# Performance work log

Hardware: AMD Instinct MI355X
Metric: run time of the kernel (lower is better)

Reference implementation:

```python
import jax, jax.numpy as jnp
import numpy as np

N, E, G = 100000, 1600000, 64
IN_DIM, EMB, HID, HEADS, OUT = 128, 128, 32, 4, 64
CAT = HID * HEADS  # 128
EPS = 1e-5
SLOPE = 0.2


def gat_conv(x, src, dst, W, a_src, a_dst, bias):
    # x: [N, F_in]; W: [HEADS*HID, F_in]; a_*: [1, HEADS, HID]; bias: [HEADS*HID]
    h = (x @ W.T).reshape(N, HEADS, HID)
    s_src = (h * a_src).sum(-1)  # [N, HEADS]
    s_dst = (h * a_dst).sum(-1)
    e = jax.nn.leaky_relu(s_src[src] + s_dst[dst], SLOPE)  # [Etot, HEADS]
    m = jax.ops.segment_max(e, dst, num_segments=N)
    p = jnp.exp(e - m[dst])
    denom = jax.ops.segment_sum(p, dst, num_segments=N)
    alpha = p / denom[dst]  # softmax over incoming edges per dst node
    out = jax.ops.segment_sum(h[src] * alpha[:, :, None], dst, num_segments=N)
    return out.reshape(N, CAT) + bias


def graph_norm(x, batch, w, b, mean_scale):
    cnt = jax.ops.segment_sum(jnp.ones((N,), x.dtype), batch, num_segments=G)[:, None]
    mean = jax.ops.segment_sum(x, batch, num_segments=G) / cnt  # [G, C]
    sub = x - mean_scale * mean[batch]
    var = jax.ops.segment_sum(sub * sub, batch, num_segments=G) / cnt
    inv = 1.0 / jnp.sqrt(var + EPS)
    return w * sub * inv[batch] + b


def setup_inputs() -> dict:
    key = jax.random.key(0)
    ks = jax.random.split(key, 20)
    g = lambda k, shape, s: jax.random.normal(k, shape, dtype=jnp.float32) * s
    inp = {
        'x': g(ks[0], (N, IN_DIM), 1.0),
        'edge_index': jax.random.randint(ks[1], (2, E), 0, N, dtype=jnp.int64 if jax.config.read('jax_enable_x64') else jnp.int32),
        'batch': jnp.sort(jax.random.randint(ks[2], (N,), 0, G)),
        'enc_w': g(ks[3], (EMB, IN_DIM), 0.08),
        'enc_b': jnp.zeros((EMB,), jnp.float32),
        'w1': g(ks[4], (HEADS * HID, EMB), 0.08),
        'att_src1': g(ks[5], (1, HEADS, HID), 0.15),
        'att_dst1': g(ks[6], (1, HEADS, HID), 0.15),
        'b1': jnp.zeros((CAT,), jnp.float32),
        'n1_w': jnp.ones((CAT,), jnp.float32),
        'n1_b': jnp.zeros((CAT,), jnp.float32),
        'n1_ms': jnp.ones((CAT,), jnp.float32),
        'w2': g(ks[7], (HEADS * HID, CAT), 0.08),
        'att_src2': g(ks[8], (1, HEADS, HID), 0.15),
        'att_dst2': g(ks[9], (1, HEADS, HID), 0.15),
        'b2': jnp.zeros((CAT,), jnp.float32),
        'n2_w': jnp.ones((CAT,), jnp.float32),
        'n2_b': jnp.zeros((CAT,), jnp.float32),
        'n2_ms': jnp.ones((CAT,), jnp.float32),
        'fc_w': g(ks[10], (OUT, CAT), 0.08),
        'fc_b': jnp.zeros((OUT,), jnp.float32),
    }
    return inp


def reference(x, edge_index, batch, enc_w, enc_b, w1, att_src1, att_dst1, b1,
              n1_w, n1_b, n1_ms, w2, att_src2, att_dst2, b2, n2_w, n2_b, n2_ms,
              fc_w, fc_b):
    # PyG GATConv adds self-loops by default
    loops = jnp.arange(N, dtype=edge_index.dtype)
    src = jnp.concatenate([edge_index[0], loops])
    dst = jnp.concatenate([edge_index[1], loops])

    h = x @ enc_w.T + enc_b
    h = jax.nn.elu(gat_conv(h, src, dst, w1, att_src1, att_dst1, b1))
    h = graph_norm(h, batch, n1_w, n1_b, n1_ms)  # dropout = identity (eval)
    h = jax.nn.elu(gat_conv(h, src, dst, w2, att_src2, att_dst2, b2))
    h = graph_norm(h, batch, n2_w, n2_b, n2_ms)
    pooled = jax.ops.segment_max(h, batch, num_segments=G)  # global_max_pool
    return pooled @ fc_w.T + fc_b  # out_dim != 1 -> no sigmoid
```

## Files before the change

### kernel.cpp

```cpp
#include <hip/hip_runtime.h>
#include <hip/hip_bf16.h>

#define SLOPE 0.2f
#define EPS_GN 1e-5f
#define APITCH 136
#define NBUCK 391

typedef __attribute__((ext_vector_type(8))) short bfrag;
typedef __attribute__((ext_vector_type(4))) float ffrag;

__device__ __forceinline__ float lrelu(float v) { return v > 0.f ? v : SLOPE * v; }
__device__ __forceinline__ short f2bs(float v) {
    __hip_bfloat16 h = __float2bfloat16(v);
    return *reinterpret_cast<short*>(&h);
}
__device__ __forceinline__ float blo(unsigned int u) { return __uint_as_float(u << 16); }
__device__ __forceinline__ float bhi(unsigned int u) { return __uint_as_float(u & 0xffff0000u); }


__global__ void __launch_bounds__(256) bucket_hist(
    const int* __restrict__ ei, int* __restrict__ bhist,
    const float* __restrict__ enc_w, const float* __restrict__ enc_b,
    const float* __restrict__ w1, const float* __restrict__ w2,
    unsigned short* __restrict__ WT1b, unsigned short* __restrict__ WT2b,
    float* __restrict__ bc1, float* __restrict__ bc2, int E, int N) {
    __shared__ int h[NBUCK];
    __shared__ float w1row[128];
    int t = threadIdx.x, bid = blockIdx.x;
    for (int i = t; i < NBUCK; i += 256) h[i] = 0;
    bool prep = (bid < 128) && (t < 128);
    if (prep) w1row[t] = w1[bid * 128 + t];
    __syncthreads();
    int base = bid * 4096;
#pragma unroll
    for (int s = 0; s < 16; ++s) {
        int e = base + s * 256 + t;
        if (e < E + N) {
            int dst = (e < E) ? ei[E + e] : (e - E);
            atomicAdd(&h[dst >> 8], 1);
        }
    }
    if (prep) {
        float acc = 0.f;
        for (int j = 0; j < 128; ++j)
            acc = fmaf(w1row[j], enc_w[j * 128 + t], acc);
        WT1b[bid * 128 + t] = (unsigned short)f2bs(acc);
        WT2b[bid * 128 + t] = (unsigned short)f2bs(w2[bid * 128 + t]);
        if (t == 0) {
            float b = 0.f;
            for (int j = 0; j < 128; ++j) b += w1row[j] * enc_b[j];
            bc1[bid] = b;
            bc2[bid] = 0.f;
        }
    }
    __syncthreads();
    for (int i = t; i < NBUCK; i += 256)
        if (h[i]) atomicAdd(&bhist[i], h[i]);
}

__global__ void bucket_scan(const int* __restrict__ bhist,
                            int* __restrict__ bbase, int* __restrict__ bcur) {
    __shared__ int sh[512];
    int t = threadIdx.x;
    int v = (t < NBUCK) ? bhist[t] : 0;
    sh[t] = v;
    __syncthreads();
    for (int off = 1; off < 512; off <<= 1) {
        int add = (t >= off) ? sh[t - off] : 0;
        __syncthreads();
        sh[t] += add;
        __syncthreads();
    }
    if (t < NBUCK) {
        bbase[t] = sh[t] - v;
        bcur[t] = sh[t] - v;
    }
}

__global__ void __launch_bounds__(256) bucket_scatter(const int* __restrict__ ei,
                                                      int* __restrict__ bcur,
                                                      unsigned int* __restrict__ staging,
                                                      int E, int N) {
    __shared__ int h[NBUCK];
    __shared__ int lb[NBUCK];
    for (int i = threadIdx.x; i < NBUCK; i += 256) h[i] = 0;
    __syncthreads();
    int base = blockIdx.x * 4096;
    int srcv[16], dstv[16];
#pragma unroll
    for (int s = 0; s < 16; ++s) {
        int e = base + s * 256 + threadIdx.x;
        srcv[s] = -1;
        if (e < E + N) {
            srcv[s] = (e < E) ? ei[e] : (e - E);
            dstv[s] = (e < E) ? ei[E + e] : (e - E);
            atomicAdd(&h[dstv[s] >> 8], 1);
        }
    }
    __syncthreads();
    for (int i = threadIdx.x; i < NBUCK; i += 256) {
        int c = h[i];
        lb[i] = c ? atomicAdd(&bcur[i], c) : 0;
        h[i] = 0;
    }
    __syncthreads();
#pragma unroll
    for (int s = 0; s < 16; ++s) {
        if (srcv[s] >= 0) {
            int b = dstv[s] >> 8;
            int slot = atomicAdd(&h[b], 1);
            staging[lb[b] + slot] = ((unsigned int)srcv[s] << 8) | (unsigned int)(dstv[s] & 255);
        }
    }
}

__global__ void __launch_bounds__(256) bucket_finalize(
    const unsigned int* __restrict__ staging,
    const int* __restrict__ bbase, const int* __restrict__ bcur,
    int* __restrict__ rowp, int* __restrict__ esrc, int N, int Etot) {
    int b = blockIdx.x, t = threadIdx.x;
    __shared__ int h[256], sc[256];
    h[t] = 0;
    __syncthreads();
    int s0 = bbase[b], s1 = bcur[b];
    for (int j = s0 + t; j < s1; j += 256)
        atomicAdd(&h[staging[j] & 255], 1);
    __syncthreads();
    int d = h[t];
    sc[t] = d;
    __syncthreads();
    for (int off = 1; off < 256; off <<= 1) {
        int add = (t >= off) ? sc[t - off] : 0;
        __syncthreads();
        sc[t] += add;
        __syncthreads();
    }
    int excl = s0 + sc[t] - d;
    int node = b * 256 + t;
    if (node < N) rowp[node] = excl;
    if (b == 0 && t == 0) rowp[N] = Etot;
    __syncthreads();
    h[t] = excl;
    __syncthreads();
    for (int j = s0 + t; j < s1; j += 256) {
        unsigned int p = staging[j];
        int pos = atomicAdd(&h[p & 255], 1);
        esrc[pos] = (int)(p >> 8);
    }
}

__global__ void __launch_bounds__(256) gemm_mfma(
    const void* __restrict__ Ain, const unsigned short* __restrict__ WTb,
    const float* __restrict__ bias, const float* __restrict__ att_src,
    const float* __restrict__ att_dst, const int* __restrict__ batch,
    const float* __restrict__ Ac, const float* __restrict__ Bc,
    unsigned int* __restrict__ H, float* __restrict__ ssrc, float* __restrict__ sdst, int N) {
    __shared__ __align__(16) short Bsh[128 * APITCH];
    __shared__ __align__(16) short Ash[64 * APITCH];
    int tid = threadIdx.x;
    int base = blockIdx.x * 64;

    int lane = tid & 63, col = lane & 15, quad = lane >> 4;
    int w = tid >> 6;
    int rowBase = w * 16;

    float2 av = *(const float2*)&att_src[lane * 2];
    float2 dv = *(const float2*)&att_dst[lane * 2];
    float bvr[8];
#pragma unroll
    for (int t = 0; t < 8; ++t) bvr[t] = bias[t * 16 + col];

    for (int idx = tid; idx < 2048; idx += 256) {
        int c = idx >> 4, k8 = (idx & 15) * 8;
        uint4 wv = ((const uint4*)WTb)[idx];
        *(uint4*)&Bsh[c * APITCH + k8] = wv;
    }
    if (Ac == nullptr) {
        const float* A = (const float*)Ain;
        for (int idx = tid; idx < 2048; idx += 256) {
            int nl = idx >> 5, k4 = (idx & 31) * 4;
            int node = base + nl;
            float4 v = make_float4(0.f, 0.f, 0.f, 0.f);
            if (node < N) v = ((const float4*)A)[node * 32 + (idx & 31)];
            *(short4*)&Ash[nl * APITCH + k4] =
                make_short4(f2bs(v.x), f2bs(v.y), f2bs(v.z), f2bs(v.w));
        }
    } else {
        const uint4* A4 = (const uint4*)Ain;
        for (int idx = tid; idx < 1024; idx += 256) {
            int nl = idx >> 4, u4 = idx & 15, k8 = u4 * 8;
            int node = base + nl;
            short o[8] = {0, 0, 0, 0, 0, 0, 0, 0};
            if (node < N) {
                uint4 hb = A4[node * 16 + u4];
                int g = batch[node];
                float4 a0 = *(const float4*)&Ac[g * 128 + k8];
                float4 a1 = *(const float4*)&Ac[g * 128 + k8 + 4];
                float4 b0 = *(const float4*)&Bc[g * 128 + k8];
                float4 b1 = *(const float4*)&Bc[g * 128 + k8 + 4];
                o[0] = f2bs(fmaf(blo(hb.x), a0.x, b0.x));
                o[1] = f2bs(fmaf(bhi(hb.x), a0.y, b0.y));
                o[2] = f2bs(fmaf(blo(hb.y), a0.z, b0.z));
                o[3] = f2bs(fmaf(bhi(hb.y), a0.w, b0.w));
                o[4] = f2bs(fmaf(blo(hb.z), a1.x, b1.x));
                o[5] = f2bs(fmaf(bhi(hb.z), a1.y, b1.y));
                o[6] = f2bs(fmaf(blo(hb.w), a1.z, b1.z));
                o[7] = f2bs(fmaf(bhi(hb.w), a1.w, b1.w));
            }
            *(bfrag*)&Ash[nl * APITCH + k8] = *(bfrag*)o;
        }
    }
    __syncthreads();

    bfrag afr[4];
#pragma unroll
    for (int s = 0; s < 4; ++s)
        afr[s] = *(const bfrag*)&Ash[(rowBase + col) * APITCH + s * 32 + quad * 8];

    ffrag acc[8];
#pragma unroll
    for (int t = 0; t < 8; ++t) acc[t] = (ffrag){0.f, 0.f, 0.f, 0.f};

#pragma unroll
    for (int t = 0; t < 8; ++t) {
#pragma unroll
        for (int s = 0; s < 4; ++s) {
            bfrag bfr = *(const bfrag*)&Bsh[(t * 16 + col) * APITCH + s * 32 + quad * 8];
            acc[t] = __builtin_amdgcn_mfma_f32_16x16x32_bf16(afr[s], bfr, acc[t], 0, 0, 0);
        }
    }

#pragma unroll
    for (int t = 0; t < 8; ++t) {
        int ch = t * 16 + col;
        float bv = bvr[t];
#pragma unroll
        for (int r = 0; r < 4; ++r)
            Ash[(rowBase + quad * 4 + r) * APITCH + ch] = f2bs(acc[t][r] + bv);
    }
    __syncthreads();

    for (int r = 0; r < 16; ++r) {
        int node = base + rowBase + r;
        unsigned int hb = *(const unsigned int*)&Ash[(rowBase + r) * APITCH + lane * 2];
        float hx = blo(hb);
        float hy = bhi(hb);
        float vs = hx * av.x + hy * av.y;
        float vd = hx * dv.x + hy * dv.y;
#pragma unroll
        for (int off = 8; off; off >>= 1) {
            vs += __shfl_xor(vs, off, 16);
            vd += __shfl_xor(vd, off, 16);
        }
        if (node < N) {
            H[node * 64 + lane] = hb;
            if ((lane & 15) == 0) {
                int h = lane >> 4;
                ssrc[node * 4 + h] = vs;
                sdst[node * 4 + h] = vd;
            }
        }
    }
}

__global__ void __launch_bounds__(256) agg_kernel(
    const int* __restrict__ row, const int* __restrict__ esrc,
    const float* __restrict__ ssrc, const float* __restrict__ sdst,
    const uint4* __restrict__ H4, const float* __restrict__ bias,
    uint4* __restrict__ out, int N) {
    int n = (blockIdx.x * 256 + threadIdx.x) >> 6;
    int lane = threadIdx.x & 63;
    if (n >= N) return;
    int slot = lane >> 4, li = lane & 15, head = li >> 2;
    int beg = row[n], end = row[n + 1];
    int last = end - 1;
    float sdh = sdst[n * 4 + head];

    float num[8] = {0.f, 0.f, 0.f, 0.f, 0.f, 0.f, 0.f, 0.f};
    float den = 0.f;
    for (int ebase = beg; ebase < end; ebase += 20) {
        int sv[5];
        float av[5];
        uint4 hv[5];
        bool ok[5];
#pragma unroll
        for (int j = 0; j < 5; ++j) {
            int e = ebase + slot + 4 * j;
            ok[j] = (e < end);
            sv[j] = esrc[min(e, last)];
        }
#pragma unroll
        for (int j = 0; j < 5; ++j) {
            av[j] = ssrc[sv[j] * 4 + head];
            hv[j] = H4[sv[j] * 16 + li];
        }
        __builtin_amdgcn_sched_barrier(0);
#pragma unroll
        for (int j = 0; j < 5; ++j) {
            float al = ok[j] ? __expf(lrelu(av[j] + sdh)) : 0.f;
            den += al;
            num[0] = fmaf(al, blo(hv[j].x), num[0]);
            num[1] = fmaf(al, bhi(hv[j].x), num[1]);
            num[2] = fmaf(al, blo(hv[j].y), num[2]);
            num[3] = fmaf(al, bhi(hv[j].y), num[3]);
            num[4] = fmaf(al, blo(hv[j].z), num[4]);
            num[5] = fmaf(al, bhi(hv[j].z), num[5]);
            num[6] = fmaf(al, blo(hv[j].w), num[6]);
            num[7] = fmaf(al, bhi(hv[j].w), num[7]);
        }
    }
    den += __shfl_xor(den, 16);
    den += __shfl_xor(den, 32);
#pragma unroll
    for (int j = 0; j < 8; ++j) {
        num[j] += __shfl_xor(num[j], 16);
        num[j] += __shfl_xor(num[j], 32);
    }
    if (slot == 0) {
        float rh = 1.f / den;
        int c0 = li * 8;
        unsigned int o[4];
#pragma unroll
        for (int p = 0; p < 4; ++p) {
            float v0 = fmaf(num[2 * p], rh, bias[c0 + 2 * p]);
            float v1 = fmaf(num[2 * p + 1], rh, bias[c0 + 2 * p + 1]);
            v0 = v0 > 0.f ? v0 : __expf(v0) - 1.f;
            v1 = v1 > 0.f ? v1 : __expf(v1) - 1.f;
            o[p] = ((unsigned int)(unsigned short)f2bs(v0)) |
                   (((unsigned int)(unsigned short)f2bs(v1)) << 16);
        }
        out[n * 16 + li] = make_uint4(o[0], o[1], o[2], o[3]);
    }
}

template <int POOL>
__global__ void __launch_bounds__(256) stats_kernel(
    const uint4* __restrict__ X4, const int* __restrict__ batch,
    float* __restrict__ part, int N) {
    __shared__ float red[16][16][9];
    int t = threadIdx.x, u4 = t & 15, rg = t >> 4;
    int base = blockIdx.x * 64;
    int g0 = batch[base];

    float s[2][8] = {}, q[2][8] = {};
    float mx[2][8], mn[2][8];
#pragma unroll
    for (int st = 0; st < 2; ++st)
#pragma unroll
        for (int p = 0; p < 8; ++p) { mx[st][p] = -3e38f; mn[st][p] = 3e38f; }

#pragma unroll
    for (int rr = 0; rr < 4; ++rr) {
        int node = base + rg + rr * 16;
        if (node < N) {
            uint4 hb = X4[node * 16 + u4];
            int st = (batch[node] != g0) ? 1 : 0;
            float vv[8] = {blo(hb.x), bhi(hb.x), blo(hb.y), bhi(hb.y),
                           blo(hb.z), bhi(hb.z), blo(hb.w), bhi(hb.w)};
#pragma unroll
            for (int p = 0; p < 8; ++p) {
                s[st][p] += vv[p];
                q[st][p] += vv[p] * vv[p];
                if (POOL) {
                    mx[st][p] = fmaxf(mx[st][p], vv[p]);
                    mn[st][p] = fminf(mn[st][p], vv[p]);
                }
            }
        }
    }

    int uu = t >> 3, ch = t & 7;
    float rs[2] = {0.f, 0.f}, rq[2] = {0.f, 0.f};
    float rmx[2] = {-3e38f, -3e38f}, rmn[2] = {3e38f, 3e38f};
    for (int st = 0; st < 2; ++st) {
#pragma unroll
        for (int p = 0; p < 8; ++p) red[rg][u4][p] = s[st][p];
        __syncthreads();
        if (t < 128) { float a = 0.f; for (int r2 = 0; r2 < 16; ++r2) a += red[r2][uu][ch]; rs[st] = a; }
        __syncthreads();
#pragma unroll
        for (int p = 0; p < 8; ++p) red[rg][u4][p] = q[st][p];
        __syncthreads();
        if (t < 128) { float a = 0.f; for (int r2 = 0; r2 < 16; ++r2) a += red[r2][uu][ch]; rq[st] = a; }
        __syncthreads();
        if (POOL) {
#pragma unroll
            for (int p = 0; p < 8; ++p) red[rg][u4][p] = mx[st][p];
            __syncthreads();
            if (t < 128) { float a = -3e38f; for (int r2 = 0; r2 < 16; ++r2) a = fmaxf(a, red[r2][uu][ch]); rmx[st] = a; }
            __syncthreads();
#pragma unroll
            for (int p = 0; p < 8; ++p) red[rg][u4][p] = mn[st][p];
            __syncthreads();
            if (t < 128) { float a = 3e38f; for (int r2 = 0; r2 < 16; ++r2) a = fminf(a, red[r2][uu][ch]); rmn[st] = a; }
            __syncthreads();
        }
    }
    if (t < 128) {
        float* pb = part + (size_t)blockIdx.x * 8 * 128;
        pb[0 * 128 + t] = rs[0];
        pb[1 * 128 + t] = rq[0];
        pb[2 * 128 + t] = rs[1];
        pb[3 * 128 + t] = rq[1];
        if (POOL) {
            pb[4 * 128 + t] = rmx[0];
            pb[5 * 128 + t] = rmn[0];
            pb[6 * 128 + t] = rmx[1];
            pb[7 * 128 + t] = rmn[1];
        }
    }
}

__global__ void reduce_coef0(const float* __restrict__ part,
                             const int* __restrict__ batch, int N,
                             const float* __restrict__ w, const float* __restrict__ b,
                             const float* __restrict__ ms,
                             float* __restrict__ Ac, float* __restrict__ Bc) {
    __shared__ int sh2[2];
    int g = blockIdx.x, c = threadIdx.x;
    if (c < 2) {
        int key = g + c;
        int lo = 0, hi = N;
        while (lo < hi) { int m = (lo + hi) >> 1; if (batch[m] < key) lo = m + 1; else hi = m; }
        sh2[c] = lo;
    }
    __syncthreads();
    int sidx = sh2[0], eidx = sh2[1];
    float cnt = (float)(eidx - sidx);
    if (cnt < 0.5f) {
        Ac[g * 128 + c] = 0.f;
        Bc[g * 128 + c] = 0.f;
        return;
    }
    int b0 = sidx >> 6, b1 = (eidx - 1) >> 6;
    float s = 0.f, q = 0.f;
    for (int bb = b0; bb <= b1; ++bb) {
        int g0b = batch[bb << 6];
        int qoff;
        bool take;
        if (g0b == g) { qoff = 0; take = true; }
        else {
            int g1b = batch[min((bb << 6) + 63, N - 1)];
            take = (g1b == g);
            qoff = 2;
        }
        if (take) {
            const float* pb = part + (size_t)bb * 8 * 128;
            s += pb[qoff * 128 + c];
            q += pb[(qoff + 1) * 128 + c];
        }
    }
    float mean = s / cnt;
    float msv = ms[c];
    float var = q / cnt - msv * (2.f - msv) * mean * mean;
    var = fmaxf(var, 0.f);
    float inv = rsqrtf(var + EPS_GN);
    float a = w[c] * inv;
    float bb2 = b[c] - msv * mean * a;
    Ac[g * 128 + c] = a;
    Bc[g * 128 + c] = bb2;
}

__global__ void rc_fc(const float* __restrict__ part,
                      const int* __restrict__ batch, int N,
                      const float* __restrict__ w, const float* __restrict__ b,
                      const float* __restrict__ ms,
                      const float* __restrict__ fcw,
                      const float* __restrict__ fcb,
                      float* __restrict__ out) {
    __shared__ int sh2[2];
    __shared__ float prow[128];
    int g = blockIdx.x, c = threadIdx.x;
    if (c < 2) {
        int key = g + c;
        int lo = 0, hi = N;
        while (lo < hi) { int m = (lo + hi) >> 1; if (batch[m] < key) lo = m + 1; else hi = m; }
        sh2[c] = lo;
    }
    __syncthreads();
    int sidx = sh2[0], eidx = sh2[1];
    float cnt = (float)(eidx - sidx);
    float pooledv = 0.f;
    if (cnt >= 0.5f) {
        int b0 = sidx >> 6, b1 = (eidx - 1) >> 6;
        float s = 0.f, q = 0.f, M = -3e38f, m = 3e38f;
        for (int bb = b0; bb <= b1; ++bb) {
            int g0b = batch[bb << 6];
            int qoff;
            bool take;
            if (g0b == g) { qoff = 0; take = true; }
            else {
                int g1b = batch[min((bb << 6) + 63, N - 1)];
                take = (g1b == g);
                qoff = 2;
            }
            if (take) {
                const float* pb = part + (size_t)bb * 8 * 128;
                s += pb[qoff * 128 + c];
                q += pb[(qoff + 1) * 128 + c];
                M = fmaxf(M, pb[(4 + qoff) * 128 + c]);
                m = fminf(m, pb[(5 + qoff) * 128 + c]);
            }
        }
        float mean = s / cnt;
        float msv = ms[c];
        float var = q / cnt - msv * (2.f - msv) * mean * mean;
        var = fmaxf(var, 0.f);
        float inv = rsqrtf(var + EPS_GN);
        float a = w[c] * inv;
        float bb2 = b[c] - msv * mean * a;
        pooledv = (a >= 0.f) ? fmaf(a, M, bb2) : fmaf(a, m, bb2);
    }
    prow[c] = pooledv;
    __syncthreads();
    if (c < 64) {
        float acc = fcb[c];
        for (int k = 0; k < 128; ++k)
            acc = fmaf(prow[k], fcw[c * 128 + k], acc);
        out[g * 64 + c] = acc;
    }
}

extern "C" void kernel_launch(void* const* d_in, const int* in_sizes, int n_in,
                              void* d_out, int out_size, void* d_ws, size_t ws_size,
                              hipStream_t stream) {
    const float* x     = (const float*)d_in[0];
    const int* ei      = (const int*)d_in[1];
    const int* batch   = (const int*)d_in[2];
    const float* enc_w = (const float*)d_in[3];
    const float* enc_b = (const float*)d_in[4];
    const float* w1    = (const float*)d_in[5];
    const float* as1   = (const float*)d_in[6];
    const float* ad1   = (const float*)d_in[7];
    const float* b1    = (const float*)d_in[8];
    const float* n1w   = (const float*)d_in[9];
    const float* n1b   = (const float*)d_in[10];
    const float* n1ms  = (const float*)d_in[11];
    const float* w2    = (const float*)d_in[12];
    const float* as2   = (const float*)d_in[13];
    const float* ad2   = (const float*)d_in[14];
    const float* b2    = (const float*)d_in[15];
    const float* n2w   = (const float*)d_in[16];
    const float* n2b   = (const float*)d_in[17];
    const float* n2ms  = (const float*)d_in[18];
    const float* fcw   = (const float*)d_in[19];
    const float* fcb   = (const float*)d_in[20];
    float* out = (float*)d_out;

    int N = in_sizes[2];
    int E = in_sizes[1] / 2;
    int Etot = E + N;
    int SB = (N + 63) / 64;

    char* ws = (char*)d_ws;
    size_t off = 0;
    auto take = [&](size_t bytes) {
        char* p = ws + off;
        off = (off + bytes + 255) & ~(size_t)255;
        return p;
    };
    unsigned short* WT1b = (unsigned short*)take(128 * 128 * 2);
    unsigned short* WT2b = (unsigned short*)take(128 * 128 * 2);
    float* bc1 = (float*)take(512);
    float* bc2 = (float*)take(512);
    float* ssrc = (float*)take((size_t)N * 16);
    float* sdst = (float*)take((size_t)N * 16);
    int* rowp   = (int*)take((size_t)(N + 1) * 4);
    int* esrc   = (int*)take((size_t)Etot * 4);
    unsigned int* staging = (unsigned int*)take((size_t)Etot * 4);
    int* bbase  = (int*)take(512 * 4);
    int* bcur   = (int*)take(512 * 4);
    int* bhist  = (int*)take(512 * 4);
    unsigned int* H = (unsigned int*)take((size_t)N * 256);
    unsigned int* AG = (unsigned int*)take((size_t)N * 256);
    float* Ac   = (float*)take(64 * 128 * 4);
    float* Bc   = (float*)take(64 * 128 * 4);
    float* part = (float*)take((size_t)SB * 8 * 128 * 4);
    if (off > ws_size) return;

    int EB = (Etot + 4095) / 4096;

    hipMemsetAsync(bhist, 0, 512 * 4, stream);

    bucket_hist<<<EB, 256, 0, stream>>>(ei, bhist, enc_w, enc_b, w1, w2,
                                        WT1b, WT2b, bc1, bc2, E, N);
    bucket_scan<<<1, 512, 0, stream>>>(bhist, bbase, bcur);
    bucket_scatter<<<EB, 256, 0, stream>>>(ei, bcur, staging, E, N);
    bucket_finalize<<<NBUCK, 256, 0, stream>>>(staging, bbase, bcur, rowp, esrc, N, Etot);

    gemm_mfma<<<(N + 63) / 64, 256, 0, stream>>>(x, WT1b, bc1, as1, ad1, batch,
                                                 nullptr, nullptr, H, ssrc, sdst, N);
    agg_kernel<<<(N + 3) / 4, 256, 0, stream>>>(rowp, esrc, ssrc, sdst,
                                                (const uint4*)H, b1, (uint4*)AG, N);
    stats_kernel<0><<<SB, 256, 0, stream>>>((const uint4*)AG, batch, part, N);
    reduce_coef0<<<64, 128, 0, stream>>>(part, batch, N, n1w, n1b, n1ms, Ac, Bc);

    gemm_mfma<<<(N + 63) / 64, 256, 0, stream>>>(AG, WT2b, bc2, as2, ad2, batch,
                                                 Ac, Bc, H, ssrc, sdst, N);
    agg_kernel<<<(N + 3) / 4, 256, 0, stream>>>(rowp, esrc, ssrc, sdst,
                                                (const uint4*)H, b2, (uint4*)AG, N);
    stats_kernel<1><<<SB, 256, 0, stream>>>((const uint4*)AG, batch, part, N);
    rc_fc<<<64, 128, 0, stream>>>(part, batch, N, n2w, n2b, n2ms, fcw, fcb, out);
}
```

Before: 441.8 us.

## Fuse GAT aggregation with graph-norm statistics and skip final feature write

Merges the per-node attention aggregation kernel with the per-block graph-norm statistics kernel. Each block now handles 64 nodes, keeps the bf16 outputs in shared memory and reduces sum, sum-of-squares and max/min from there, so the aggregated features are not re-read from global memory. The second layer no longer writes its aggregated features at all, since only the statistics and pooled values are needed. The trade-off is fewer, larger blocks, with each wave processing 16 nodes in sequence, which can reduce the parallelism available to hide gather latency.

```diff
diff --git a/kernel.cpp b/kernel.cpp
--- a/kernel.cpp
+++ b/kernel.cpp
@@ -263,150 +263,121 @@
     }
 }
 
-__global__ void __launch_bounds__(256) agg_kernel(
+template <int POOL, int WROUT>
+__global__ void __launch_bounds__(256) agg_stats(
     const int* __restrict__ row, const int* __restrict__ esrc,
     const float* __restrict__ ssrc, const float* __restrict__ sdst,
     const uint4* __restrict__ H4, const float* __restrict__ bias,
-    uint4* __restrict__ out, int N) {
-    int n = (blockIdx.x * 256 + threadIdx.x) >> 6;
-    int lane = threadIdx.x & 63;
-    if (n >= N) return;
+    uint4* __restrict__ out, const int* __restrict__ batch,
+    float* __restrict__ part, int N) {
+    __shared__ unsigned int rows[64][64];
+    __shared__ int bsh[64];
+    int tid = threadIdx.x;
+    int lane = tid & 63, w = tid >> 6;
     int slot = lane >> 4, li = lane & 15, head = li >> 2;
-    int beg = row[n], end = row[n + 1];
-    int last = end - 1;
-    float sdh = sdst[n * 4 + head];
-
-    float num[8] = {0.f, 0.f, 0.f, 0.f, 0.f, 0.f, 0.f, 0.f};
-    float den = 0.f;
-    for (int ebase = beg; ebase < end; ebase += 20) {
-        int sv[5];
-        float av[5];
-        uint4 hv[5];
-        bool ok[5];
-#pragma unroll
-        for (int j = 0; j < 5; ++j) {
-            int e = ebase + slot + 4 * j;
-            ok[j] = (e < end);
-            sv[j] = esrc[min(e, last)];
-        }
-#pragma unroll
-        for (int j = 0; j < 5; ++j) {
-            av[j] = ssrc[sv[j] * 4 + head];
-            hv[j] = H4[sv[j] * 16 + li];
-        }
-        __builtin_amdgcn_sched_barrier(0);
-#pragma unroll
-        for (int j = 0; j < 5; ++j) {
-            float al = ok[j] ? __expf(lrelu(av[j] + sdh)) : 0.f;
-            den += al;
-            num[0] = fmaf(al, blo(hv[j].x), num[0]);
-            num[1] = fmaf(al, bhi(hv[j].x), num[1]);
-            num[2] = fmaf(al, blo(hv[j].y), num[2]);
-            num[3] = fmaf(al, bhi(hv[j].y), num[3]);
-            num[4] = fmaf(al, blo(hv[j].z), num[4]);
-            num[5] = fmaf(al, bhi(hv[j].z), num[5]);
-            num[6] = fmaf(al, blo(hv[j].w), num[6]);
-            num[7] = fmaf(al, bhi(hv[j].w), num[7]);
-        }
-    }
-    den += __shfl_xor(den, 16);
-    den += __shfl_xor(den, 32);
-#pragma unroll
-    for (int j = 0; j < 8; ++j) {
-        num[j] += __shfl_xor(num[j], 16);
-        num[j] += __shfl_xor(num[j], 32);
-    }
-    if (slot == 0) {
-        float rh = 1.f / den;
-        int c0 = li * 8;
-        unsigned int o[4];
-#pragma unroll
-        for (int p = 0; p < 4; ++p) {
-            float v0 = fmaf(num[2 * p], rh, bias[c0 + 2 * p]);
-            float v1 = fmaf(num[2 * p + 1], rh, bias[c0 + 2 * p + 1]);
-            v0 = v0 > 0.f ? v0 : __expf(v0) - 1.f;
-            v1 = v1 > 0.f ? v1 : __expf(v1) - 1.f;
-            o[p] = ((unsigned int)(unsigned short)f2bs(v0)) |
-                   (((unsigned int)(unsigned short)f2bs(v1)) << 16);
-        }
-        out[n * 16 + li] = make_uint4(o[0], o[1], o[2], o[3]);
-    }
-}
-
-template <int POOL>
-__global__ void __launch_bounds__(256) stats_kernel(
-    const uint4* __restrict__ X4, const int* __restrict__ batch,
-    float* __restrict__ part, int N) {
-    __shared__ float red[16][16][9];
-    int t = threadIdx.x, u4 = t & 15, rg = t >> 4;
     int base = blockIdx.x * 64;
-    int g0 = batch[base];
-
-    float s[2][8] = {}, q[2][8] = {};
-    float mx[2][8], mn[2][8];
-#pragma unroll
-    for (int st = 0; st < 2; ++st)
-#pragma unroll
-        for (int p = 0; p < 8; ++p) { mx[st][p] = -3e38f; mn[st][p] = 3e38f; }
-
-#pragma unroll
-    for (int rr = 0; rr < 4; ++rr) {
-        int node = base + rg + rr * 16;
-        if (node < N) {
-            uint4 hb = X4[node * 16 + u4];
-            int st = (batch[node] != g0) ? 1 : 0;
-            float vv[8] = {blo(hb.x), bhi(hb.x), blo(hb.y), bhi(hb.y),
-                           blo(hb.z), bhi(hb.z), blo(hb.w), bhi(hb.w)};
-#pragma unroll
-            for (int p = 0; p < 8; ++p) {
-                s[st][p] += vv[p];
-                q[st][p] += vv[p] * vv[p];
-                if (POOL) {
-                    mx[st][p] = fmaxf(mx[st][p], vv[p]);
-                    mn[st][p] = fminf(mn[st][p], vv[p]);
+
+    if (tid < 64) bsh[tid] = (base + tid < N) ? batch[base + tid] : -1;
+
+    int c0 = li * 8;
+    float bv[8];
+#pragma unroll
+    for (int p = 0; p < 8; ++p) bv[p] = bias[c0 + p];
+
+    for (int r = 0; r < 16; ++r) {
+        int n = base + w * 16 + r;
+        if (n < N) {
+            int beg = row[n], end = row[n + 1];
+            int last = end - 1;
+            float sdh = sdst[n * 4 + head];
+
+            float num[8] = {0.f, 0.f, 0.f, 0.f, 0.f, 0.f, 0.f, 0.f};
+            float den = 0.f;
+            for (int ebase = beg; ebase < end; ebase += 20) {
+                int sv[5];
+                float av[5];
+                uint4 hv[5];
+                bool ok[5];
+#pragma unroll
+                for (int j = 0; j < 5; ++j) {
+                    int e = ebase + slot + 4 * j;
+                    ok[j] = (e < end);
+                    sv[j] = esrc[min(e, last)];
                 }
-            }
-        }
-    }
-
-    int uu = t >> 3, ch = t & 7;
-    float rs[2] = {0.f, 0.f}, rq[2] = {0.f, 0.f};
-    float rmx[2] = {-3e38f, -3e38f}, rmn[2] = {3e38f, 3e38f};
-    for (int st = 0; st < 2; ++st) {
-#pragma unroll
-        for (int p = 0; p < 8; ++p) red[rg][u4][p] = s[st][p];
-        __syncthreads();
-        if (t < 128) { float a = 0.f; for (int r2 = 0; r2 < 16; ++r2) a += red[r2][uu][ch]; rs[st] = a; }
-        __syncthreads();
-#pragma unroll
-        for (int p = 0; p < 8; ++p) red[rg][u4][p] = q[st][p];
-        __syncthreads();
-        if (t < 128) { float a = 0.f; for (int r2 = 0; r2 < 16; ++r2) a += red[r2][uu][ch]; rq[st] = a; }
-        __syncthreads();
+#pragma unroll
+                for (int j = 0; j < 5; ++j) {
+                    av[j] = ssrc[sv[j] * 4 + head];
+                    hv[j] = H4[sv[j] * 16 + li];
+                }
+                __builtin_amdgcn_sched_barrier(0);
+#pragma unroll
+                for (int j = 0; j < 5; ++j) {
+                    float al = ok[j] ? __expf(lrelu(av[j] + sdh)) : 0.f;
+                    den += al;
+                    num[0] = fmaf(al, blo(hv[j].x), num[0]);
+                    num[1] = fmaf(al, bhi(hv[j].x), num[1]);
+                    num[2] = fmaf(al, blo(hv[j].y), num[2]);
+                    num[3] = fmaf(al, bhi(hv[j].y), num[3]);
+                    num[4] = fmaf(al, blo(hv[j].z), num[4]);
+                    num[5] = fmaf(al, bhi(hv[j].z), num[5]);
+                    num[6] = fmaf(al, blo(hv[j].w), num[6]);
+                    num[7] = fmaf(al, bhi(hv[j].w), num[7]);
+                }
+            }
+            den += __shfl_xor(den, 16);
+            den += __shfl_xor(den, 32);
+#pragma unroll
+            for (int j = 0; j < 8; ++j) {
+                num[j] += __shfl_xor(num[j], 16);
+                num[j] += __shfl_xor(num[j], 32);
+            }
+            if (slot == 0) {
+                float rh = 1.f / den;
+                unsigned int o[4];
+#pragma unroll
+                for (int p = 0; p < 4; ++p) {
+                    float v0 = fmaf(num[2 * p], rh, bv[2 * p]);
+                    float v1 = fmaf(num[2 * p + 1], rh, bv[2 * p + 1]);
+                    v0 = v0 > 0.f ? v0 : __expf(v0) - 1.f;
+                    v1 = v1 > 0.f ? v1 : __expf(v1) - 1.f;
+                    o[p] = ((unsigned int)(unsigned short)f2bs(v0)) |
+                           (((unsigned int)(unsigned short)f2bs(v1)) << 16);
+                }
+                uint4 ov = make_uint4(o[0], o[1], o[2], o[3]);
+                *(uint4*)&rows[w * 16 + r][li * 4] = ov;
+                if (WROUT) out[n * 16 + li] = ov;
+            }
+        }
+    }
+    __syncthreads();
+
+    if (tid < 128) {
+        int g0 = bsh[0];
+        float s[2] = {0.f, 0.f}, q[2] = {0.f, 0.f};
+        float mx[2] = {-3e38f, -3e38f}, mn[2] = {3e38f, 3e38f};
+        for (int n2 = 0; n2 < 64; ++n2) {
+            int bvn = bsh[n2];
+            if (bvn < 0) continue;
+            unsigned int wv = rows[n2][tid >> 1];
+            float v = (tid & 1) ? bhi(wv) : blo(wv);
+            int st = (bvn != g0) ? 1 : 0;
+            s[st] += v;
+            q[st] += v * v;
+            if (POOL) {
+                mx[st] = fmaxf(mx[st], v);
+                mn[st] = fminf(mn[st], v);
+            }
+        }
+        float* pb = part + (size_t)blockIdx.x * 8 * 128;
+        pb[0 * 128 + tid] = s[0];
+        pb[1 * 128 + tid] = q[0];
+        pb[2 * 128 + tid] = s[1];
+        pb[3 * 128 + tid] = q[1];
         if (POOL) {
-#pragma unroll
-            for (int p = 0; p < 8; ++p) red[rg][u4][p] = mx[st][p];
-            __syncthreads();
-            if (t < 128) { float a = -3e38f; for (int r2 = 0; r2 < 16; ++r2) a = fmaxf(a, red[r2][uu][ch]); rmx[st] = a; }
-            __syncthreads();
-#pragma unroll
-            for (int p = 0; p < 8; ++p) red[rg][u4][p] = mn[st][p];
-            __syncthreads();
-            if (t < 128) { float a = 3e38f; for (int r2 = 0; r2 < 16; ++r2) a = fminf(a, red[r2][uu][ch]); rmn[st] = a; }
-            __syncthreads();
-        }
-    }
-    if (t < 128) {
-        float* pb = part + (size_t)blockIdx.x * 8 * 128;
-        pb[0 * 128 + t] = rs[0];
-        pb[1 * 128 + t] = rq[0];
-        pb[2 * 128 + t] = rs[1];
-        pb[3 * 128 + t] = rq[1];
-        if (POOL) {
-            pb[4 * 128 + t] = rmx[0];
-            pb[5 * 128 + t] = rmn[0];
-            pb[6 * 128 + t] = rmx[1];
-            pb[7 * 128 + t] = rmn[1];
+            pb[4 * 128 + tid] = mx[0];
+            pb[5 * 128 + tid] = mn[0];
+            pb[6 * 128 + tid] = mx[1];
+            pb[7 * 128 + tid] = mn[1];
         }
     }
 }
@@ -588,17 +559,17 @@
     bucket_scatter<<<EB, 256, 0, stream>>>(ei, bcur, staging, E, N);
     bucket_finalize<<<NBUCK, 256, 0, stream>>>(staging, bbase, bcur, rowp, esrc, N, Etot);
 
-    gemm_mfma<<<(N + 63) / 64, 256, 0, stream>>>(x, WT1b, bc1, as1, ad1, batch,
-                                                 nullptr, nullptr, H, ssrc, sdst, N);
-    agg_kernel<<<(N + 3) / 4, 256, 0, stream>>>(rowp, esrc, ssrc, sdst,
-                                                (const uint4*)H, b1, (uint4*)AG, N);
-    stats_kernel<0><<<SB, 256, 0, stream>>>((const uint4*)AG, batch, part, N);
+    gemm_mfma<<<SB, 256, 0, stream>>>(x, WT1b, bc1, as1, ad1, batch,
+                                      nullptr, nullptr, H, ssrc, sdst, N);
+    agg_stats<0, 1><<<SB, 256, 0, stream>>>(rowp, esrc, ssrc, sdst,
+                                            (const uint4*)H, b1, (uint4*)AG,
+                                            batch, part, N);
     reduce_coef0<<<64, 128, 0, stream>>>(part, batch, N, n1w, n1b, n1ms, Ac, Bc);
 
-    gemm_mfma<<<(N + 63) / 64, 256, 0, stream>>>(AG, WT2b, bc2, as2, ad2, batch,
-                                                 Ac, Bc, H, ssrc, sdst, N);
-    agg_kernel<<<(N + 3) / 4, 256, 0, stream>>>(rowp, esrc, ssrc, sdst,
-                                                (const uint4*)H, b2, (uint4*)AG, N);
-    stats_kernel<1><<<SB, 256, 0, stream>>>((const uint4*)AG, batch, part, N);
+    gemm_mfma<<<SB, 256, 0, stream>>>(AG, WT2b, bc2, as2, ad2, batch,
+                                      Ac, Bc, H, ssrc, sdst, N);
+    agg_stats<1, 0><<<SB, 256, 0, stream>>>(rowp, esrc, ssrc, sdst,
+                                            (const uint4*)H, b2, nullptr,
+                                            batch, part, N);
     rc_fc<<<64, 128, 0, stream>>>(part, batch, N, n2w, n2b, n2ms, fcw, fcb, out);
 }
```

Result: slower. 487.0 us (+10.2%).

## Merge bucket histogram and scatter into one pass using fixed-capacity bucket staging

Applied to the files above, without the earlier changes.

Removes the separate histogram pass and its scan before the scatter. Each block now claims slots in a per-bucket staging region of fixed capacity (BCAP), so the edge list is read once instead of twice and one kernel launch is dropped. The scan now runs after the scatter, and finalize reads each bucket from its own fixed-offset region. The risk is overflow if any bucket of 256 destination nodes receives more than 6144 edges. The staging buffer also grows to NBUCK*BCAP entries.

```diff
diff --git a/kernel.cpp b/kernel.cpp
--- a/kernel.cpp
+++ b/kernel.cpp
@@ -5,6 +5,7 @@
 #define EPS_GN 1e-5f
 #define APITCH 136
 #define NBUCK 391
+#define BCAP 6144
 
 typedef __attribute__((ext_vector_type(8))) short bfrag;
 typedef __attribute__((ext_vector_type(4))) float ffrag;
@@ -18,13 +19,15 @@
 __device__ __forceinline__ float bhi(unsigned int u) { return __uint_as_float(u & 0xffff0000u); }
 
 
-__global__ void __launch_bounds__(256) bucket_hist(
-    const int* __restrict__ ei, int* __restrict__ bhist,
+__global__ void __launch_bounds__(256) bucket_scatter(
+    const int* __restrict__ ei, int* __restrict__ bcur,
+    unsigned int* __restrict__ staging,
     const float* __restrict__ enc_w, const float* __restrict__ enc_b,
     const float* __restrict__ w1, const float* __restrict__ w2,
     unsigned short* __restrict__ WT1b, unsigned short* __restrict__ WT2b,
     float* __restrict__ bc1, float* __restrict__ bc2, int E, int N) {
     __shared__ int h[NBUCK];
+    __shared__ int lb[NBUCK];
     __shared__ float w1row[128];
     int t = threadIdx.x, bid = blockIdx.x;
     for (int i = t; i < NBUCK; i += 256) h[i] = 0;
@@ -32,12 +35,15 @@
     if (prep) w1row[t] = w1[bid * 128 + t];
     __syncthreads();
     int base = bid * 4096;
+    int srcv[16], dstv[16];
 #pragma unroll
     for (int s = 0; s < 16; ++s) {
         int e = base + s * 256 + t;
+        srcv[s] = -1;
         if (e < E + N) {
-            int dst = (e < E) ? ei[E + e] : (e - E);
-            atomicAdd(&h[dst >> 8], 1);
+            srcv[s] = (e < E) ? ei[e] : (e - E);
+            dstv[s] = (e < E) ? ei[E + e] : (e - E);
+            atomicAdd(&h[dstv[s] >> 8], 1);
         }
     }
     if (prep) {
@@ -54,51 +60,7 @@
         }
     }
     __syncthreads();
-    for (int i = t; i < NBUCK; i += 256)
-        if (h[i]) atomicAdd(&bhist[i], h[i]);
-}
-
-__global__ void bucket_scan(const int* __restrict__ bhist,
-                            int* __restrict__ bbase, int* __restrict__ bcur) {
-    __shared__ int sh[512];
-    int t = threadIdx.x;
-    int v = (t < NBUCK) ? bhist[t] : 0;
-    sh[t] = v;
-    __syncthreads();
-    for (int off = 1; off < 512; off <<= 1) {
-        int add = (t >= off) ? sh[t - off] : 0;
-        __syncthreads();
-        sh[t] += add;
-        __syncthreads();
-    }
-    if (t < NBUCK) {
-        bbase[t] = sh[t] - v;
-        bcur[t] = sh[t] - v;
-    }
-}
-
-__global__ void __launch_bounds__(256) bucket_scatter(const int* __restrict__ ei,
-                                                      int* __restrict__ bcur,
-                                                      unsigned int* __restrict__ staging,
-                                                      int E, int N) {
-    __shared__ int h[NBUCK];
-    __shared__ int lb[NBUCK];
-    for (int i = threadIdx.x; i < NBUCK; i += 256) h[i] = 0;
-    __syncthreads();
-    int base = blockIdx.x * 4096;
-    int srcv[16], dstv[16];
-#pragma unroll
-    for (int s = 0; s < 16; ++s) {
-        int e = base + s * 256 + threadIdx.x;
-        srcv[s] = -1;
-        if (e < E + N) {
-            srcv[s] = (e < E) ? ei[e] : (e - E);
-            dstv[s] = (e < E) ? ei[E + e] : (e - E);
-            atomicAdd(&h[dstv[s] >> 8], 1);
-        }
-    }
-    __syncthreads();
-    for (int i = threadIdx.x; i < NBUCK; i += 256) {
+    for (int i = t; i < NBUCK; i += 256) {
         int c = h[i];
         lb[i] = c ? atomicAdd(&bcur[i], c) : 0;
         h[i] = 0;
@@ -109,22 +71,39 @@
         if (srcv[s] >= 0) {
             int b = dstv[s] >> 8;
             int slot = atomicAdd(&h[b], 1);
-            staging[lb[b] + slot] = ((unsigned int)srcv[s] << 8) | (unsigned int)(dstv[s] & 255);
-        }
-    }
+            staging[(size_t)b * BCAP + lb[b] + slot] =
+                ((unsigned int)srcv[s] << 8) | (unsigned int)(dstv[s] & 255);
+        }
+    }
+}
+
+__global__ void bucket_scan(const int* __restrict__ bcnt, int* __restrict__ bbase) {
+    __shared__ int sh[512];
+    int t = threadIdx.x;
+    int v = (t < NBUCK) ? bcnt[t] : 0;
+    sh[t] = v;
+    __syncthreads();
+    for (int off = 1; off < 512; off <<= 1) {
+        int add = (t >= off) ? sh[t - off] : 0;
+        __syncthreads();
+        sh[t] += add;
+        __syncthreads();
+    }
+    if (t < NBUCK) bbase[t] = sh[t] - v;
 }
 
 __global__ void __launch_bounds__(256) bucket_finalize(
     const unsigned int* __restrict__ staging,
-    const int* __restrict__ bbase, const int* __restrict__ bcur,
+    const int* __restrict__ bbase, const int* __restrict__ bcnt,
     int* __restrict__ rowp, int* __restrict__ esrc, int N, int Etot) {
     int b = blockIdx.x, t = threadIdx.x;
     __shared__ int h[256], sc[256];
     h[t] = 0;
     __syncthreads();
-    int s0 = bbase[b], s1 = bcur[b];
-    for (int j = s0 + t; j < s1; j += 256)
-        atomicAdd(&h[staging[j] & 255], 1);
+    int cnt = bcnt[b];
+    const unsigned int* st = staging + (size_t)b * BCAP;
+    for (int j = t; j < cnt; j += 256)
+        atomicAdd(&h[st[j] & 255], 1);
     __syncthreads();
     int d = h[t];
     sc[t] = d;
@@ -135,15 +114,15 @@
         sc[t] += add;
         __syncthreads();
     }
-    int excl = s0 + sc[t] - d;
+    int excl = bbase[b] + sc[t] - d;
     int node = b * 256 + t;
     if (node < N) rowp[node] = excl;
     if (b == 0 && t == 0) rowp[N] = Etot;
     __syncthreads();
     h[t] = excl;
     __syncthreads();
-    for (int j = s0 + t; j < s1; j += 256) {
-        unsigned int p = staging[j];
+    for (int j = t; j < cnt; j += 256) {
+        unsigned int p = st[j];
         int pos = atomicAdd(&h[p & 255], 1);
         esrc[pos] = (int)(p >> 8);
     }
@@ -567,10 +546,9 @@
     float* sdst = (float*)take((size_t)N * 16);
     int* rowp   = (int*)take((size_t)(N + 1) * 4);
     int* esrc   = (int*)take((size_t)Etot * 4);
-    unsigned int* staging = (unsigned int*)take((size_t)Etot * 4);
+    unsigned int* staging = (unsigned int*)take((size_t)NBUCK * BCAP * 4);
     int* bbase  = (int*)take(512 * 4);
     int* bcur   = (int*)take(512 * 4);
-    int* bhist  = (int*)take(512 * 4);
     unsigned int* H = (unsigned int*)take((size_t)N * 256);
     unsigned int* AG = (unsigned int*)take((size_t)N * 256);
     float* Ac   = (float*)take(64 * 128 * 4);
@@ -580,23 +558,22 @@
 
     int EB = (Etot + 4095) / 4096;
 
-    hipMemsetAsync(bhist, 0, 512 * 4, stream);
-
-    bucket_hist<<<EB, 256, 0, stream>>>(ei, bhist, enc_w, enc_b, w1, w2,
-                                        WT1b, WT2b, bc1, bc2, E, N);
-    bucket_scan<<<1, 512, 0, stream>>>(bhist, bbase, bcur);
-    bucket_scatter<<<EB, 256, 0, stream>>>(ei, bcur, staging, E, N);
+    hipMemsetAsync(bcur, 0, 512 * 4, stream);
+
+    bucket_scatter<<<EB, 256, 0, stream>>>(ei, bcur, staging, enc_w, enc_b,
+                                           w1, w2, WT1b, WT2b, bc1, bc2, E, N);
+    bucket_scan<<<1, 512, 0, stream>>>(bcur, bbase);
     bucket_finalize<<<NBUCK, 256, 0, stream>>>(staging, bbase, bcur, rowp, esrc, N, Etot);
 
-    gemm_mfma<<<(N + 63) / 64, 256, 0, stream>>>(x, WT1b, bc1, as1, ad1, batch,
-                                                 nullptr, nullptr, H, ssrc, sdst, N);
+    gemm_mfma<<<SB, 256, 0, stream>>>(x, WT1b, bc1, as1, ad1, batch,
+                                      nullptr, nullptr, H, ssrc, sdst, N);
     agg_kernel<<<(N + 3) / 4, 256, 0, stream>>>(rowp, esrc, ssrc, sdst,
                                                 (const uint4*)H, b1, (uint4*)AG, N);
     stats_kernel<0><<<SB, 256, 0, stream>>>((const uint4*)AG, batch, part, N);
     reduce_coef0<<<64, 128, 0, stream>>>(part, batch, N, n1w, n1b, n1ms, Ac, Bc);
 
-    gemm_mfma<<<(N + 63) / 64, 256, 0, stream>>>(AG, WT2b, bc2, as2, ad2, batch,
-                                                 Ac, Bc, H, ssrc, sdst, N);
+    gemm_mfma<<<SB, 256, 0, stream>>>(AG, WT2b, bc2, as2, ad2, batch,
+                                      Ac, Bc, H, ssrc, sdst, N);
     agg_kernel<<<(N + 3) / 4, 256, 0, stream>>>(rowp, esrc, ssrc, sdst,
                                                 (const uint4*)H, b2, (uint4*)AG, N);
     stats_kernel<1><<<SB, 256, 0, stream>>>((const uint4*)AG, batch, part, N);
```

Measured after the change: 428.0 us. 3.1% less time.
